# Performance work log

Measured on AMD Instinct MI355X. Metric: run time of the kernel, lower is better.

Reference implementation:

```python
import jax, jax.numpy as jnp
import numpy as np

DIM = 48
HEADS = 8
DIM1 = DIM * HEADS  # 384
RED = 16


def setup_inputs() -> dict:
    key = jax.random.key(0)
    ks = jax.random.split(key, 10)
    s = 0.02
    return {
        "x": jax.random.normal(ks[0], (4, DIM, 128, 128), dtype=jnp.float32),
        "qkv_w": jax.random.normal(ks[1], (DIM1 * 4, DIM), dtype=jnp.float32) * s,
        "dw_w": jax.random.normal(ks[2], (DIM1 * 4, HEADS, 3, 3), dtype=jnp.float32) * s,  # groups=DIM*4 -> 8 in-ch per group
        "po1_w": jax.random.normal(ks[3], (DIM, DIM1), dtype=jnp.float32) * s,
        "fc1_w": jax.random.normal(ks[4], (DIM1 // RED, DIM1), dtype=jnp.float32) * s,
        "fc1_b": jnp.zeros((DIM1 // RED,), dtype=jnp.float32),
        "fc2_w": jax.random.normal(ks[5], (DIM1, DIM1 // RED), dtype=jnp.float32) * s,
        "fc2_b": jnp.zeros((DIM1,), dtype=jnp.float32),
        "temperature": jnp.ones((HEADS, 1, 1), dtype=jnp.float32),
    }


def reference(x, qkv_w, dw_w, po1_w, fc1_w, fc1_b, fc2_w, fc2_b, temperature):
    b, c, h, w = x.shape  # c == dim
    heads = temperature.shape[0]
    # 1x1 pointwise conv: dim -> dim1*4
    qkv = jnp.einsum('bchw,oc->bohw', x, qkv_w)
    # grouped 3x3 conv, groups = dim*4 (8 channels per group)
    qkv = jax.lax.conv_general_dilated(
        qkv, dw_w, window_strides=(1, 1), padding='SAME',
        feature_group_count=c * 4,
        dimension_numbers=('NCHW', 'OIHW', 'NCHW'))
    q, k, v, l = jnp.split(qkv, 4, axis=1)  # each (b, dim1, h, w)
    hw = h * w
    q = q.reshape(b, heads, c, hw)
    k = k.reshape(b, heads, c, hw)
    v = v.reshape(b, heads, c, hw)
    # ChannelAttention on l: note it returns fc2_out * sigmoid(fc2_out)
    avg = jnp.mean(l, axis=(2, 3))  # (b, dim1)
    y = jax.nn.relu(avg @ fc1_w.T + fc1_b)
    y = y @ fc2_w.T + fc2_b  # (b, dim1)
    L = (y * jax.nn.sigmoid(y))[:, :, None, None]  # (b, dim1, 1, 1)
    # L2-normalize over spatial (last) axis, torch eps=1e-12
    q = q / jnp.clip(jnp.linalg.norm(q, axis=-1, keepdims=True), 1e-12)
    k = k / jnp.clip(jnp.linalg.norm(k, axis=-1, keepdims=True), 1e-12)
    # channel-wise attention: (b, heads, c, c)
    attn = jnp.einsum('bhcn,bhdn->bhcd', q, k) * temperature
    attn = jax.nn.softmax(attn, axis=-1)
    out = jnp.einsum('bhcd,bhdn->bhcn', attn, v).reshape(b, heads * c, h, w)
    out = L + out
    out = jnp.einsum('bchw,oc->bohw', out, po1_w) + x
    return out
```

## Files before the change

kernel.cpp:

```cpp
#include <hip/hip_runtime.h>
#include <cstdint>

#define BB 4
#define CC 48
#define HW 16384
#define D1 384
#define HEADS 8

typedef unsigned short ushort_t;
typedef __attribute__((ext_vector_type(8))) short short8;
typedef __attribute__((ext_vector_type(4))) float f32x4;

__device__ __forceinline__ float bf2f(ushort_t u){
  union{uint32_t i; float f;} v; v.i = ((uint32_t)u)<<16; return v.f;
}
__device__ __forceinline__ ushort_t f2bf(float f){
  union{float f; uint32_t i;} v; v.f=f;
  uint32_t x = v.i;
  uint32_t r = (x + 0x7fff + ((x>>16)&1)) >> 16;
  return (ushort_t)r;
}

__global__ __launch_bounds__(256) void k_wf(const float* __restrict__ dw,
                                            const float* __restrict__ qw,
                                            ushort_t* __restrict__ wfp,
                                            float* __restrict__ qn2){
  int oc = blockIdx.x, tid = threadIdx.x;
  if(oc < 12){ int i = oc*256 + tid; if(i < 3072) qn2[i] = 0.f; }
  for(int kk=tid; kk<448; kk+=256){
    int t = kk/48, c = kk - t*48;
    float s = 0.f;
    if(t < 9){
      #pragma unroll
      for(int j=0;j<8;j++)
        s += dw[(size_t)oc*72 + j*9 + t] * qw[(size_t)((oc>>3)*8 + j)*48 + c];
    }
    wfp[(size_t)oc*448 + kk] = f2bf(s);
  }
}

__global__ __launch_bounds__(256) void k_xstats(const float* __restrict__ x,
                                                float* __restrict__ xst){
  int ch = blockIdx.x, b = blockIdx.y;
  const float* p = x + ((size_t)b*CC + ch)*HW;
  int tid = threadIdx.x;
  float T=0,R0=0,R1=0,C0=0,C1=0;
  for(int i=tid;i<HW;i+=256){
    float v = p[i];
    T += v;
    if(i<128)      R0 += v;
    if(i>=16256)   R1 += v;
    int xc = i & 127;
    if(xc==0)      C0 += v;
    if(xc==127)    C1 += v;
  }
  __shared__ float red[20];
  for(int off=32;off;off>>=1){
    T  += __shfl_down(T,off);  R0 += __shfl_down(R0,off); R1 += __shfl_down(R1,off);
    C0 += __shfl_down(C0,off); C1 += __shfl_down(C1,off);
  }
  int wv = tid>>6, ln = tid&63;
  if(ln==0){ red[wv]=T; red[4+wv]=R0; red[8+wv]=R1; red[12+wv]=C0; red[16+wv]=C1; }
  __syncthreads();
  if(tid==0){
    float* o = xst + ((size_t)b*CC + ch)*9;
    o[0]=red[0]+red[1]+red[2]+red[3];
    o[1]=red[4]+red[5]+red[6]+red[7];
    o[2]=red[8]+red[9]+red[10]+red[11];
    o[3]=red[12]+red[13]+red[14]+red[15];
    o[4]=red[16]+red[17]+red[18]+red[19];
    o[5]=p[0]; o[6]=p[127]; o[7]=p[16256]; o[8]=p[16383];
  }
}

__global__ __launch_bounds__(256) void k_xpose(const float* __restrict__ x,
                                               ushort_t* __restrict__ xb16){
  int gy = blockIdx.x;
  int b  = blockIdx.y;
  ushort_t* orow = xb16 + ((size_t)b*130 + gy)*130*48;
  int tid = threadIdx.x;
  if(gy==0 || gy==129){
    short8 z = {0,0,0,0,0,0,0,0};
    for(int u=tid; u<780; u+=256) *(short8*)(orow + u*8) = z;
    return;
  }
  __shared__ float xl[48*128];
  const float* xr = x + (size_t)b*CC*HW + (size_t)(gy-1)*128;
  for(int i=tid;i<6144;i+=256){
    int c=i>>7, p=i&127;
    xl[c*128+p] = xr[(size_t)c*HW + p];
  }
  __syncthreads();
  for(int u=tid; u<780; u+=256){
    int gx = u/6, s = u-gx*6;
    ushort_t tmp[8];
    if(gx==0||gx==129){
      #pragma unroll
      for(int j=0;j<8;j++) tmp[j]=0;
    } else {
      #pragma unroll
      for(int j=0;j<8;j++) tmp[j] = f2bf(xl[(s*8+j)*128 + (gx-1)]);
    }
    *(short8*)(orow + (size_t)u*8) = *(short8*)tmp;
  }
}

#define HROWC 64
__global__ __launch_bounds__(256,3) void k_conv(const ushort_t* __restrict__ xb16,
                                                const ushort_t* __restrict__ wfp,
                                                ushort_t* __restrict__ qkvd){
  __shared__ __align__(16) ushort_t xs[180*HROWC];
  int tid  = threadIdx.x;
  int wave = tid>>6, lane = tid&63;
  int quad = lane>>4, mrow = lane&15;
  int mhalf = wave>>1, nhalf = wave&1;
  int tile = blockIdx.x;
  int ty0 = (tile>>3)*8, tx0 = (tile&7)*16;
  int ocb = blockIdx.y*128 + mhalf*64;
  int b   = blockIdx.z;

  const ushort_t* xh = xb16 + ((size_t)b*16900 + (size_t)ty0*130 + tx0)*48;
  for(int u=tid; u<1944; u+=256){
    int r = u/6, g = u - r*6;
    int hy = r/18, hx = r - hy*18;
    short8 v = *(const short8*)(xh + ((size_t)hy*130 + hx)*48 + g*8);
    *(short8*)(xs + r*HROWC + ((g ^ (r&7))<<3)) = v;
  }
  __syncthreads();

  int rb[4];
  #pragma unroll
  for(int nt=0;nt<4;nt++) rb[nt] = (nhalf*4+nt+1)*18 + mrow + 1;

  const ushort_t* Abase = wfp + (size_t)(ocb + mrow)*448 + quad*8;
  f32x4 Cacc[4][4];
  #pragma unroll
  for(int mt=0;mt<4;mt++)
    #pragma unroll
    for(int nt=0;nt<4;nt++) Cacc[mt][nt] = (f32x4){0.f,0.f,0.f,0.f};

  short8 Ac[4], An[4];
  #pragma unroll
  for(int mt=0;mt<4;mt++) Ac[mt] = *(const short8*)(Abase + (size_t)mt*16*448);

  #pragma unroll
  for(int chunk=0; chunk<14; chunk++){
    if(chunk < 13){
      #pragma unroll
      for(int mt=0;mt<4;mt++)
        An[mt] = *(const short8*)(Abase + (size_t)mt*16*448 + (chunk+1)*32);
    }
    int kq = chunk*32 + quad*8;
    int t  = kq/48;
    int c  = kq - t*48;
    int tc = (t<9) ? t : 8;
    int dyq = tc/3;
    int drow = dyq*18 + (tc - dyq*3) - 19;
    int g = c>>3;
    short8 Bf[4];
    #pragma unroll
    for(int nt=0;nt<4;nt++){
      int r = rb[nt] + drow;
      Bf[nt] = *(const short8*)(xs + r*HROWC + ((g ^ (r&7))<<3));
    }
    #pragma unroll
    for(int mt=0;mt<4;mt++)
      #pragma unroll
      for(int nt=0;nt<4;nt++)
        Cacc[mt][nt] = __builtin_amdgcn_mfma_f32_16x16x32_bf16(Ac[mt], Bf[nt], Cacc[mt][nt], 0,0,0);
    #pragma unroll
    for(int mt=0;mt<4;mt++) Ac[mt] = An[mt];
  }

  #pragma unroll
  for(int mt=0;mt<4;mt++){
    #pragma unroll
    for(int nt=0;nt<4;nt++){
      int py = nhalf*4 + nt;
      int gpos = (ty0+py)*128 + tx0 + mrow;
      #pragma unroll
      for(int r=0;r<4;r++){
        int oc = ocb + mt*16 + quad*4 + r;
        qkvd[((size_t)b*1152 + oc)*HW + gpos] = f2bf(Cacc[mt][nt][r]);
      }
    }
  }
}

__global__ __launch_bounds__(256,3) void k_S(const ushort_t* __restrict__ qkvd,
                                             float* __restrict__ Spart,
                                             float* __restrict__ qn2){
  __shared__ __align__(16) ushort_t qk[96*264];
  int tid = threadIdx.x;
  int blk = blockIdx.x, h = blockIdx.y, b = blockIdx.z;
  int wave = tid>>6, lane = tid&63;
  int quad = lane>>4, mrow = lane&15;
  const ushort_t* qb = qkvd + ((size_t)b*1152 + h*48)*HW;
  const ushort_t* kb = qb + (size_t)384*HW;

  f32x4 accS[3][3], accq[3], acck[3];
  #pragma unroll
  for(int mt=0;mt<3;mt++){
    accq[mt] = (f32x4){0.f,0.f,0.f,0.f};
    acck[mt] = (f32x4){0.f,0.f,0.f,0.f};
    #pragma unroll
    for(int nt=0;nt<3;nt++) accS[mt][nt] = (f32x4){0.f,0.f,0.f,0.f};
  }

  for(int half=0; half<2; half++){
    int p0 = blk*512 + half*256;
    __syncthreads();
    for(int u=tid; u<3072; u+=256){
      int ch = u>>5, px = u&31;
      const ushort_t* src = ((ch<48) ? qb + (size_t)ch*HW
                                     : kb + (size_t)(ch-48)*HW) + p0 + px*8;
      *(short8*)(qk + ch*264 + px*8) = *(const short8*)src;
    }
    __syncthreads();
    #pragma unroll
    for(int ks=0; ks<2; ks++){
      int koff = wave*64 + ks*32 + quad*8;
      short8 Aq[3], Bk[3];
      #pragma unroll
      for(int mt=0;mt<3;mt++) Aq[mt] = *(const short8*)(qk + (mt*16+mrow)*264 + koff);
      #pragma unroll
      for(int nt=0;nt<3;nt++) Bk[nt] = *(const short8*)(qk + (48+nt*16+mrow)*264 + koff);
      #pragma unroll
      for(int mt=0;mt<3;mt++){
        accq[mt] = __builtin_amdgcn_mfma_f32_16x16x32_bf16(Aq[mt], Aq[mt], accq[mt], 0,0,0);
        acck[mt] = __builtin_amdgcn_mfma_f32_16x16x32_bf16(Bk[mt], Bk[mt], acck[mt], 0,0,0);
        #pragma unroll
        for(int nt=0;nt<3;nt++)
          accS[mt][nt] = __builtin_amdgcn_mfma_f32_16x16x32_bf16(Aq[mt], Bk[nt], accS[mt][nt], 0,0,0);
      }
    }
  }
  __syncthreads();
  float* scr = (float*)qk;
  #pragma unroll
  for(int mt=0;mt<3;mt++)
    #pragma unroll
    for(int nt=0;nt<3;nt++)
      #pragma unroll
      for(int r=0;r<4;r++)
        scr[wave*2304 + (mt*16+quad*4+r)*48 + nt*16 + mrow] = accS[mt][nt][r];
  __syncthreads();
  float* outp = Spart + ((size_t)((b*HEADS+h)*32 + blk))*2304;
  for(int idx=tid; idx<2304; idx+=256)
    outp[idx] = scr[idx] + scr[2304+idx] + scr[4608+idx] + scr[6912+idx];
  int rr = mrow - (quad<<2);
  #pragma unroll
  for(int r=0;r<4;r++){
    if(rr == r){
      #pragma unroll
      for(int mt=0;mt<3;mt++){
        atomicAdd(qn2 + (size_t)b*D1 + h*48 + mt*16 + mrow, accq[mt][r]);
        atomicAdd(qn2 + 1536 + (size_t)b*D1 + h*48 + mt*16 + mrow, acck[mt][r]);
      }
    }
  }
}

__global__ __launch_bounds__(384) void k_mlp(const float* __restrict__ xst,
                                             const float* __restrict__ qw,
                                             const float* __restrict__ dw,
                                             const float* __restrict__ fc1w,
                                             const float* __restrict__ fc1b,
                                             const float* __restrict__ fc2w,
                                             const float* __restrict__ fc2b,
                                             const float* __restrict__ po1,
                                             float* __restrict__ constv){
  int b = blockIdx.x, tid = threadIdx.x;
  __shared__ float xsl[432];
  __shared__ float lst[3456];
  __shared__ float avg[384];
  __shared__ float y1[24];
  __shared__ float Lb[384];
  for(int i=tid;i<432;i+=384) xsl[i] = xst[(size_t)b*432 + i];
  __syncthreads();
  {
    float st[9];
    #pragma unroll
    for(int s=0;s<9;s++) st[s]=0.f;
    const float* w = qw + (size_t)(1152+tid)*48;
    for(int c=0;c<48;c++){
      float wv = w[c];
      #pragma unroll
      for(int s=0;s<9;s++) st[s] += wv*xsl[c*9+s];
    }
    #pragma unroll
    for(int s=0;s<9;s++) lst[tid*9+s] = st[s];
  }
  __syncthreads();
  {
    int base = tid & ~7;
    const float* ls = &lst[base*9];
    float s = 0.f;
    #pragma unroll
    for(int i=0;i<8;i++){
      float T=ls[i*9+0],R0=ls[i*9+1],R1=ls[i*9+2],C0=ls[i*9+3],C1=ls[i*9+4];
      float c00=ls[i*9+5],c0W=ls[i*9+6],cH0=ls[i*9+7],cHW=ls[i*9+8];
      const float* wp = dw + (size_t)(1152+tid)*72 + i*9;
      #pragma unroll
      for(int dy=0;dy<3;dy++){
        float rm = (dy==0)?R1:((dy==2)?R0:0.f);
        #pragma unroll
        for(int dx=0;dx<3;dx++){
          float cm = (dx==0)?C1:((dx==2)?C0:0.f);
          float corner = 0.f;
          if(dy==0&&dx==0)corner=cHW;
          if(dy==0&&dx==2)corner=cH0;
          if(dy==2&&dx==0)corner=c0W;
          if(dy==2&&dx==2)corner=c00;
          s += wp[dy*3+dx]*(T-rm-cm+corner);
        }
      }
    }
    avg[tid] = s*(1.f/16384.f);
  }
  __syncthreads();
  if(tid<24){
    float s = fc1b[tid];
    const float* w = fc1w + (size_t)tid*384;
    for(int c=0;c<384;c++) s += w[c]*avg[c];
    y1[tid] = fmaxf(s,0.f);
  }
  __syncthreads();
  {
    float s = fc2b[tid];
    const float* w = fc2w + (size_t)tid*24;
    #pragma unroll
    for(int j=0;j<24;j++) s += w[j]*y1[j];
    Lb[tid] = s/(1.f+__expf(-s));
  }
  __syncthreads();
  if(tid<48){
    const float* w = po1 + (size_t)tid*384;
    float s = 0.f;
    for(int c=0;c<384;c++) s += w[c]*Lb[c];
    constv[b*48+tid] = s;
  }
}

__global__ __launch_bounds__(256) void k_attn(const float* __restrict__ Spart,
                                              const float* __restrict__ qn2,
                                              const float* __restrict__ temp,
                                              const float* __restrict__ po1,
                                              ushort_t* __restrict__ m2o){
  int h = blockIdx.x, b = blockIdx.y, tid = threadIdx.x;
  __shared__ float att[2304];
  __shared__ float nq[48], nk[48];
  const float* kn2 = qn2 + 1536;
  if(tid<48)      nq[tid]    = fmaxf(sqrtf(qn2[(size_t)b*D1 + h*48 + tid]),    1e-12f);
  else if(tid<96) nk[tid-48] = fmaxf(sqrtf(kn2[(size_t)b*D1 + h*48 + tid-48]), 1e-12f);
  __syncthreads();
  float tmp = temp[h];
  const float* Sp = Spart + ((size_t)(b*HEADS+h)*32)*2304;
  for(int idx=tid; idx<2304; idx+=256){
    float s = 0.f;
    for(int blk=0;blk<32;blk++) s += Sp[(size_t)blk*2304 + idx];
    int c = idx/48, d = idx - c*48;
    att[idx] = s*tmp/(nq[c]*nk[d]);
  }
  __syncthreads();
  if(tid<48){
    float* row = &att[tid*48];
    float m = -1e30f;
    for(int d=0;d<48;d++) m = fmaxf(m,row[d]);
    float s = 0.f;
    for(int d=0;d<48;d++){ float e=__expf(row[d]-m); row[d]=e; s+=e; }
    float inv = 1.f/s;
    for(int d=0;d<48;d++) row[d]*=inv;
  }
  __syncthreads();
  for(int idx=tid; idx<2304; idx+=256){
    int d = idx/48, o = idx - d*48;
    float s = 0.f;
    for(int c=0;c<48;c++) s += po1[(size_t)o*D1 + h*48 + c]*att[c*48+d];
    m2o[((size_t)b*48 + o)*D1 + h*48 + d] = f2bf(s);
  }
}

#define FROW 40
__global__ __launch_bounds__(256) void k_final(const ushort_t* __restrict__ qkvd,
                                               const ushort_t* __restrict__ m2o,
                                               const float* __restrict__ constv,
                                               const float* __restrict__ x,
                                               float* __restrict__ out){
  __shared__ __align__(16) ushort_t vsT[256*FROW];
  int tid = threadIdx.x;
  int wave = tid>>6, lane = tid&63;
  int quad = lane>>4, mrow = lane&15;
  int pos0 = blockIdx.x*256;
  int b = blockIdx.y;
  const ushort_t* vb = qkvd + ((size_t)b*1152 + 768)*HW + pos0;
  const ushort_t* Ab = m2o + (size_t)b*48*D1;
  f32x4 acc[3][4];
  #pragma unroll
  for(int mt=0;mt<3;mt++)
    #pragma unroll
    for(int nt=0;nt<4;nt++) acc[mt][nt] = (f32x4){0.f,0.f,0.f,0.f};
  int baddr[4];
  #pragma unroll
  for(int nt=0;nt<4;nt++){
    int p = wave*64 + nt*16 + mrow;
    baddr[nt] = p*FROW + ((quad ^ ((p>>3)&3))<<3);
  }
  for(int ck=0; ck<12; ck++){
    __syncthreads();
    {
      int p = tid;
      #pragma unroll
      for(int g=0; g<4; g++){
        const ushort_t* src = vb + (size_t)(ck*32 + g*8)*HW + p;
        ushort_t tmp[8];
        #pragma unroll
        for(int j=0;j<8;j++) tmp[j] = src[(size_t)j*HW];
        *(short8*)(vsT + p*FROW + ((g ^ ((p>>3)&3))<<3)) = *(short8*)tmp;
      }
    }
    __syncthreads();
    short8 Af[3], Bf[4];
    #pragma unroll
    for(int mt=0;mt<3;mt++)
      Af[mt] = *(const short8*)(Ab + (size_t)(mt*16+mrow)*D1 + ck*32 + quad*8);
    #pragma unroll
    for(int nt=0;nt<4;nt++) Bf[nt] = *(const short8*)(vsT + baddr[nt]);
    #pragma unroll
    for(int mt=0;mt<3;mt++)
      #pragma unroll
      for(int nt=0;nt<4;nt++)
        acc[mt][nt] = __builtin_amdgcn_mfma_f32_16x16x32_bf16(Af[mt], Bf[nt], acc[mt][nt], 0,0,0);
  }
  const float* xb = x + (size_t)b*CC*HW + pos0;
  float* ob = out + (size_t)b*CC*HW + pos0;
  #pragma unroll
  for(int mt=0;mt<3;mt++)
    #pragma unroll
    for(int nt=0;nt<4;nt++){
      int p = wave*64 + nt*16 + mrow;
      #pragma unroll
      for(int r=0;r<4;r++){
        int o = mt*16 + quad*4 + r;
        ob[(size_t)o*HW + p] = xb[(size_t)o*HW + p] + constv[b*48+o] + acc[mt][nt][r];
      }
    }
}

extern "C" void kernel_launch(void* const* d_in, const int* in_sizes, int n_in,
                              void* d_out, int out_size, void* d_ws, size_t ws_size,
                              hipStream_t stream){
  const float* x    = (const float*)d_in[0];
  const float* qw   = (const float*)d_in[1];
  const float* dw   = (const float*)d_in[2];
  const float* po1  = (const float*)d_in[3];
  const float* fc1w = (const float*)d_in[4];
  const float* fc1b = (const float*)d_in[5];
  const float* fc2w = (const float*)d_in[6];
  const float* fc2b = (const float*)d_in[7];
  const float* temp = (const float*)d_in[8];
  float* out = (float*)d_out;
  char* ws = (char*)d_ws;

  ushort_t* qkvd   = (ushort_t*)(ws);
  float*    Spart  = (float*)(ws + 150994944);
  ushort_t* xb16   = (ushort_t*)(ws + 150994944);
  float*    qn2    = (float*)(ws + 160432128);
  float*    xst    = (float*)(ws + 160444416);
  float*    constv = (float*)(ws + 160451328);
  ushort_t* m2o    = (ushort_t*)(ws + 160452096);
  ushort_t* wfp    = (ushort_t*)(ws + 160599552);

  k_wf    <<<dim3(1152),         256, 0, stream>>>(dw, qw, wfp, qn2);
  k_xstats<<<dim3(48,BB),        256, 0, stream>>>(x, xst);
  k_xpose <<<dim3(130,BB),       256, 0, stream>>>(x, xb16);
  k_conv  <<<dim3(128,9,BB),     256, 0, stream>>>(xb16, wfp, qkvd);
  k_S     <<<dim3(32,HEADS,BB),  256, 0, stream>>>(qkvd, Spart, qn2);
  k_mlp   <<<dim3(BB),           384, 0, stream>>>(xst, qw, dw, fc1w, fc1b, fc2w, fc2b, po1, constv);
  k_attn  <<<dim3(HEADS,BB),     256, 0, stream>>>(Spart, qn2, temp, po1, m2o);
  k_final <<<dim3(64,BB),        256, 0, stream>>>(qkvd, m2o, constv, x, out);
}
```

Before: 351.9 us.

## Fuse x statistics into transpose, double-buffer final GEMM, raise conv occupancy

The separate x-statistics kernel is removed and its sums are computed inside the transpose kernel from the row already in shared memory, using atomics into a zeroed buffer. The zeroing range in k_wf grows so the xst region is cleared. The final projection kernel now uses 128-position tiles with a double-buffered, vectorized V staging and a new swizzle, giving more blocks and overlapping loads with MFMA work. The conv kernel's launch bound asks for higher occupancy, which may force register spills. Atomic accumulation makes the float sums order-dependent, and the new zeroing only works if xst sits directly after qn2 in the workspace.

```diff
diff --git a/kernel.cpp b/kernel.cpp
--- a/kernel.cpp
+++ b/kernel.cpp
@@ -26,7 +26,7 @@
                                             ushort_t* __restrict__ wfp,
                                             float* __restrict__ qn2){
   int oc = blockIdx.x, tid = threadIdx.x;
-  if(oc < 12){ int i = oc*256 + tid; if(i < 3072) qn2[i] = 0.f; }
+  if(oc < 19){ int i = oc*256 + tid; if(i < 4800) qn2[i] = 0.f; }
   for(int kk=tid; kk<448; kk+=256){
     int t = kk/48, c = kk - t*48;
     float s = 0.f;
@@ -39,42 +39,9 @@
   }
 }
 
-__global__ __launch_bounds__(256) void k_xstats(const float* __restrict__ x,
-                                                float* __restrict__ xst){
-  int ch = blockIdx.x, b = blockIdx.y;
-  const float* p = x + ((size_t)b*CC + ch)*HW;
-  int tid = threadIdx.x;
-  float T=0,R0=0,R1=0,C0=0,C1=0;
-  for(int i=tid;i<HW;i+=256){
-    float v = p[i];
-    T += v;
-    if(i<128)      R0 += v;
-    if(i>=16256)   R1 += v;
-    int xc = i & 127;
-    if(xc==0)      C0 += v;
-    if(xc==127)    C1 += v;
-  }
-  __shared__ float red[20];
-  for(int off=32;off;off>>=1){
-    T  += __shfl_down(T,off);  R0 += __shfl_down(R0,off); R1 += __shfl_down(R1,off);
-    C0 += __shfl_down(C0,off); C1 += __shfl_down(C1,off);
-  }
-  int wv = tid>>6, ln = tid&63;
-  if(ln==0){ red[wv]=T; red[4+wv]=R0; red[8+wv]=R1; red[12+wv]=C0; red[16+wv]=C1; }
-  __syncthreads();
-  if(tid==0){
-    float* o = xst + ((size_t)b*CC + ch)*9;
-    o[0]=red[0]+red[1]+red[2]+red[3];
-    o[1]=red[4]+red[5]+red[6]+red[7];
-    o[2]=red[8]+red[9]+red[10]+red[11];
-    o[3]=red[12]+red[13]+red[14]+red[15];
-    o[4]=red[16]+red[17]+red[18]+red[19];
-    o[5]=p[0]; o[6]=p[127]; o[7]=p[16256]; o[8]=p[16383];
-  }
-}
-
 __global__ __launch_bounds__(256) void k_xpose(const float* __restrict__ x,
-                                               ushort_t* __restrict__ xb16){
+                                               ushort_t* __restrict__ xb16,
+                                               float* __restrict__ xst){
   int gy = blockIdx.x;
   int b  = blockIdx.y;
   ushort_t* orow = xb16 + ((size_t)b*130 + gy)*130*48;
@@ -103,10 +70,23 @@
     }
     *(short8*)(orow + (size_t)u*8) = *(short8*)tmp;
   }
+  if(tid < 48){
+    const float* row = &xl[tid*128];
+    float a0=0,a1=0,a2=0,a3=0;
+    #pragma unroll 8
+    for(int p=0;p<128;p+=4){ a0+=row[p]; a1+=row[p+1]; a2+=row[p+2]; a3+=row[p+3]; }
+    float s = (a0+a1)+(a2+a3);
+    float* o = xst + ((size_t)b*48 + tid)*9;
+    atomicAdd(&o[0], s);
+    atomicAdd(&o[3], row[0]);
+    atomicAdd(&o[4], row[127]);
+    if(gy==1)  { o[1]=s; o[5]=row[0]; o[6]=row[127]; }
+    if(gy==128){ o[2]=s; o[7]=row[0]; o[8]=row[127]; }
+  }
 }
 
 #define HROWC 64
-__global__ __launch_bounds__(256,3) void k_conv(const ushort_t* __restrict__ xb16,
+__global__ __launch_bounds__(256,5) void k_conv(const ushort_t* __restrict__ xb16,
                                                 const ushort_t* __restrict__ wfp,
                                                 ushort_t* __restrict__ qkvd){
   __shared__ __align__(16) ushort_t xs[180*HROWC];
@@ -381,64 +361,70 @@
   }
 }
 
-#define FROW 40
-__global__ __launch_bounds__(256) void k_final(const ushort_t* __restrict__ qkvd,
-                                               const ushort_t* __restrict__ m2o,
-                                               const float* __restrict__ constv,
-                                               const float* __restrict__ x,
-                                               float* __restrict__ out){
-  __shared__ __align__(16) ushort_t vsT[256*FROW];
+#define FROW2 40
+__global__ __launch_bounds__(256,3) void k_final(const ushort_t* __restrict__ qkvd,
+                                                 const ushort_t* __restrict__ m2o,
+                                                 const float* __restrict__ constv,
+                                                 const float* __restrict__ x,
+                                                 float* __restrict__ out){
+  __shared__ __align__(16) ushort_t vT[2][128*FROW2];
   int tid = threadIdx.x;
   int wave = tid>>6, lane = tid&63;
   int quad = lane>>4, mrow = lane&15;
-  int pos0 = blockIdx.x*256;
+  int pos0 = blockIdx.x*128;
   int b = blockIdx.y;
   const ushort_t* vb = qkvd + ((size_t)b*1152 + 768)*HW + pos0;
   const ushort_t* Ab = m2o + (size_t)b*48*D1;
-  f32x4 acc[3][4];
+  f32x4 acc[3][2];
   #pragma unroll
   for(int mt=0;mt<3;mt++)
     #pragma unroll
-    for(int nt=0;nt<4;nt++) acc[mt][nt] = (f32x4){0.f,0.f,0.f,0.f};
-  int baddr[4];
-  #pragma unroll
-  for(int nt=0;nt<4;nt++){
-    int p = wave*64 + nt*16 + mrow;
-    baddr[nt] = p*FROW + ((quad ^ ((p>>3)&3))<<3);
-  }
+    for(int nt=0;nt<2;nt++) acc[mt][nt] = (f32x4){0.f,0.f,0.f,0.f};
+
+  auto stage = [&](int ck, int buf){
+    #pragma unroll
+    for(int s=0;s<2;s++){
+      int unit = tid + s*256;
+      int ch = unit>>4, pg = unit&15, p0 = pg*8;
+      int chg = ch>>3, cl = ch&7;
+      short8 v = *(const short8*)(vb + (size_t)(ck*32+ch)*HW + p0);
+      ushort_t tmp[8]; *(short8*)tmp = v;
+      #pragma unroll
+      for(int i=0;i<8;i++){
+        int p = p0+i;
+        int sl = (chg ^ (p&3) ^ ((p>>3)&3)) & 3;
+        vT[buf][p*FROW2 + (sl<<3) + cl] = tmp[i];
+      }
+    }
+  };
+  stage(0,0);
+  __syncthreads();
   for(int ck=0; ck<12; ck++){
-    __syncthreads();
-    {
-      int p = tid;
-      #pragma unroll
-      for(int g=0; g<4; g++){
-        const ushort_t* src = vb + (size_t)(ck*32 + g*8)*HW + p;
-        ushort_t tmp[8];
-        #pragma unroll
-        for(int j=0;j<8;j++) tmp[j] = src[(size_t)j*HW];
-        *(short8*)(vsT + p*FROW + ((g ^ ((p>>3)&3))<<3)) = *(short8*)tmp;
-      }
-    }
-    __syncthreads();
-    short8 Af[3], Bf[4];
+    if(ck<11) stage(ck+1, (ck+1)&1);
+    short8 Af[3], Bf[2];
     #pragma unroll
     for(int mt=0;mt<3;mt++)
       Af[mt] = *(const short8*)(Ab + (size_t)(mt*16+mrow)*D1 + ck*32 + quad*8);
     #pragma unroll
-    for(int nt=0;nt<4;nt++) Bf[nt] = *(const short8*)(vsT + baddr[nt]);
+    for(int nt=0;nt<2;nt++){
+      int p = wave*32 + nt*16 + mrow;
+      int sl = (quad ^ (p&3) ^ ((p>>3)&3)) & 3;
+      Bf[nt] = *(const short8*)(&vT[ck&1][p*FROW2 + (sl<<3)]);
+    }
     #pragma unroll
     for(int mt=0;mt<3;mt++)
       #pragma unroll
-      for(int nt=0;nt<4;nt++)
+      for(int nt=0;nt<2;nt++)
         acc[mt][nt] = __builtin_amdgcn_mfma_f32_16x16x32_bf16(Af[mt], Bf[nt], acc[mt][nt], 0,0,0);
+    __syncthreads();
   }
   const float* xb = x + (size_t)b*CC*HW + pos0;
   float* ob = out + (size_t)b*CC*HW + pos0;
   #pragma unroll
   for(int mt=0;mt<3;mt++)
     #pragma unroll
-    for(int nt=0;nt<4;nt++){
-      int p = wave*64 + nt*16 + mrow;
+    for(int nt=0;nt<2;nt++){
+      int p = wave*32 + nt*16 + mrow;
       #pragma unroll
       for(int r=0;r<4;r++){
         int o = mt*16 + quad*4 + r;
@@ -472,11 +458,10 @@
   ushort_t* wfp    = (ushort_t*)(ws + 160599552);
 
   k_wf    <<<dim3(1152),         256, 0, stream>>>(dw, qw, wfp, qn2);
-  k_xstats<<<dim3(48,BB),        256, 0, stream>>>(x, xst);
-  k_xpose <<<dim3(130,BB),       256, 0, stream>>>(x, xb16);
+  k_xpose <<<dim3(130,BB),       256, 0, stream>>>(x, xb16, xst);
   k_conv  <<<dim3(128,9,BB),     256, 0, stream>>>(xb16, wfp, qkvd);
   k_S     <<<dim3(32,HEADS,BB),  256, 0, stream>>>(qkvd, Spart, qn2);
   k_mlp   <<<dim3(BB),           384, 0, stream>>>(xst, qw, dw, fc1w, fc1b, fc2w, fc2b, po1, constv);
   k_attn  <<<dim3(HEADS,BB),     256, 0, stream>>>(Spart, qn2, temp, po1, m2o);
-  k_final <<<dim3(64,BB),        256, 0, stream>>>(qkvd, m2o, constv, x, out);
-}
+  k_final <<<dim3(128,BB),       256, 0, stream>>>(qkvd, m2o, constv, x, out);
+}
```

Measured after the change: 565.8 us. 1.61x slower.
